# Kernel optimization log

Hardware: AMD Instinct MI355X
Metric: run time of the kernel (lower is better)

The kernel has to match this reference:

```python
import jax, jax.numpy as jnp
import numpy as np

EMBED_DIM = 256
NUM_HEADS = 8
HEAD_DIM = EMBED_DIM // NUM_HEADS


def setup_inputs() -> dict:
    key0 = jax.random.key(0)
    ks = jax.random.split(key0, 12)
    B, T, S, E = 4, 256, 16384, EMBED_DIM
    inv = 1.0 / np.sqrt(E)
    inputs = {
        "query": jax.random.normal(ks[0], (B, T, E), dtype=jnp.float32),
        "key": jax.random.normal(ks[1], (B, S, E), dtype=jnp.float32),
        "value": jax.random.normal(ks[2], (B, S, E), dtype=jnp.float32),
        "mask": jax.random.uniform(ks[3], (B, T, S), dtype=jnp.float32),
        # nn.MultiheadAttention in-projection (split into q/k/v parts) and out-projection
        "Wq": jax.random.uniform(ks[4], (E, E), jnp.float32, -inv, inv),
        "bq": jnp.zeros((E,), jnp.float32),
        "Wk": jax.random.uniform(ks[5], (E, E), jnp.float32, -inv, inv),
        "bk": jnp.zeros((E,), jnp.float32),
        "Wv": jax.random.uniform(ks[6], (E, E), jnp.float32, -inv, inv),
        "bv": jnp.zeros((E,), jnp.float32),
        "Wo": jax.random.uniform(ks[7], (E, E), jnp.float32, -inv, inv),
        "bo": jnp.zeros((E,), jnp.float32),
        # fixed default scaling factors (num_heads must be 8)
        "scaling_factors": jnp.asarray([32.0, 32.0, 16.0, 16.0, 8.0, 8.0, 4.0, 4.0], jnp.float32),
    }
    return inputs


def reference(query, key, value, mask, Wq, bq, Wk, bk, Wv, bv, Wo, bo, scaling_factors):
    B, T, E = query.shape
    S = key.shape[1]
    H, D = NUM_HEADS, HEAD_DIM
    # input projections (torch Linear convention: x @ W.T + b)
    q = (query @ Wq.T + bq).reshape(B, T, H, D).transpose(0, 2, 1, 3)  # [B,H,T,D]
    k = (key @ Wk.T + bk).reshape(B, S, H, D).transpose(0, 2, 1, 3)    # [B,H,S,D]
    v = (value @ Wv.T + bv).reshape(B, S, H, D).transpose(0, 2, 1, 3)  # [B,H,S,D]
    scale = 1.0 / jnp.sqrt(jnp.asarray(D, query.dtype))
    scores = jnp.einsum("bhtd,bhsd->bhts", q * scale, k)               # [B,H,T,S]
    # per-head scaled soft mask added as attention bias
    bias = mask[:, None, :, :] * scaling_factors[None, :, None, None]  # [B,H,T,S]
    attn = jax.nn.softmax(scores + bias, axis=-1)
    out = jnp.einsum("bhts,bhsd->bhtd", attn, v)                       # [B,H,T,D]
    out = out.transpose(0, 2, 1, 3).reshape(B, T, E)
    return out @ Wo.T + bo
```

## Files before the change

kernel.cpp:

```cpp
#include <hip/hip_runtime.h>

#define B_ 4
#define T_ 256
#define S_ 16384
#define E_ 256
#define H_ 8
#define D_ 32

typedef _Float16 f16;
typedef _Float16 f16x2 __attribute__((ext_vector_type(2)));
typedef _Float16 f16x4 __attribute__((ext_vector_type(4)));
typedef _Float16 f16x8 __attribute__((ext_vector_type(8)));
typedef float f32x4 __attribute__((ext_vector_type(4)));

typedef const __attribute__((address_space(1))) void* gas_t;
typedef __attribute__((address_space(3))) void* las_t;

#define FENCE() asm volatile("" ::: "memory")

__device__ __forceinline__ void gload_lds16(const void* g, void* l) {
    __builtin_amdgcn_global_load_lds((gas_t)g, (las_t)l, 16, 0, 0);
}

__device__ __forceinline__ f16x2 cvt_pk_f16(float a, float b) {
    return __builtin_bit_cast(f16x2, __builtin_amdgcn_cvt_pkrtz(a, b));
}

__device__ __forceinline__ f16x8 pack8(float4 a, float4 b) {
    f16x2 p0 = cvt_pk_f16(a.x, a.y), p1 = cvt_pk_f16(a.z, a.w);
    f16x2 p2 = cvt_pk_f16(b.x, b.y), p3 = cvt_pk_f16(b.z, b.w);
    return (f16x8){p0[0], p0[1], p1[0], p1[1], p2[0], p2[1], p3[0], p3[1]};
}

#define LOG2E 1.4426950408889634f

template <bool OUT16>
__device__ __forceinline__ void qproj32_body(
    f16* SMEM, const float* __restrict__ in, const float* __restrict__ w,
    const float* __restrict__ bias, void* __restrict__ outp, int bid, float oscale)
{
    f16 (*As)[264] = (f16(*)[264])SMEM;
    f16 (*Bs)[264] = (f16(*)[264])(SMEM + 32 * 264);
    int tid = threadIdx.x;
    int wq = tid >> 6, ln = tid & 63, g = ln >> 4, lc = ln & 15;
    int row0 = (bid & 31) * 32;
    int n0 = (bid >> 5) * 32;
    {
        int r = tid >> 3, q0 = (tid & 7) * 32;
        const float* ip = in + (size_t)(row0 + r) * 256 + q0;
        #pragma unroll
        for (int i = 0; i < 4; i++) {
            float4 v0 = *(const float4*)(ip + i * 8);
            float4 v1 = *(const float4*)(ip + i * 8 + 4);
            *(f16x8*)&As[r][q0 + i * 8] = pack8(v0, v1);
        }
        const float* wp = w + (size_t)(n0 + r) * 256 + q0;
        #pragma unroll
        for (int i = 0; i < 4; i++) {
            float4 v0 = *(const float4*)(wp + i * 8);
            float4 v1 = *(const float4*)(wp + i * 8 + 4);
            *(f16x8*)&Bs[r][q0 + i * 8] = pack8(v0, v1);
        }
    }
    __syncthreads();
    int mi = wq >> 1, ni = wq & 1;
    f32x4 acc = {0.f, 0.f, 0.f, 0.f};
    #pragma unroll
    for (int ks = 0; ks < 8; ks++) {
        f16x8 a = *(const f16x8*)&As[mi * 16 + lc][ks * 32 + g * 8];
        f16x8 bf = *(const f16x8*)&Bs[ni * 16 + lc][ks * 32 + g * 8];
        acc = __builtin_amdgcn_mfma_f32_16x16x32_f16(a, bf, acc, 0, 0, 0);
    }
    int n = n0 + ni * 16 + lc;
    float bv = bias[n];
    #pragma unroll
    for (int r = 0; r < 4; r++) {
        int row = row0 + mi * 16 + g * 4 + r;
        float val = (acc[r] + bv) * oscale;
        if (OUT16) ((f16*)outp)[(size_t)row * 256 + n] = (f16)val;
        else       ((float*)outp)[(size_t)row * 256 + n] = val;
    }
}

__global__ __launch_bounds__(256) void pre_kernel(
    const float* __restrict__ Wk, const float* __restrict__ Wv,
    f16* __restrict__ Wk16, f16* __restrict__ Wv16,
    const float* __restrict__ query, const float* __restrict__ Wq,
    const float* __restrict__ bq, f16* __restrict__ q16, float qscale)
{
    __shared__ __align__(16) f16 SMEM[16896];
    int bx = blockIdx.x;
    if (bx < 128) {
        const float* src = bx < 64 ? Wk : Wv;
        f16* dst = bx < 64 ? Wk16 : Wv16;
        int i = ((bx & 63) * 256 + threadIdx.x) * 4;
        float4 v = *(const float4*)(src + i);
        f16x4 h = {(f16)v.x, (f16)v.y, (f16)v.z, (f16)v.w};
        *(f16x4*)(dst + i) = h;
    } else {
        qproj32_body<true>(SMEM, query, Wq, bq, q16, bx - 128, qscale);
    }
}

template <int MODE>
__device__ __forceinline__ void proj8_body(
    char* SMEM, const float* __restrict__ in, const f16* __restrict__ w16,
    const float* __restrict__ bias, f16* __restrict__ out, int bx)
{
    f16 (*As)[128][40] = (f16(*)[128][40])SMEM;
    f16* Bs = (f16*)(SMEM + 20480);
    int tid = threadIdx.x;
    int wq = tid >> 6, ln = tid & 63, g = ln >> 4, lc = ln & 15;
    int mh = wq >> 2, nq = wq & 3;
    int row0 = bx * 128;

    f32x4 acc[4][4];
    #pragma unroll
    for (int i = 0; i < 4; i++)
        #pragma unroll
        for (int j = 0; j < 4; j++) acc[i][j] = (f32x4){0.f, 0.f, 0.f, 0.f};

    int am = tid >> 2, akq = (tid & 3) << 3;
    const float* abase = in + (size_t)(row0 + am) * 256 + akq;

    float4 Ar[2][2];
    auto issueA = [&](int t) {
        const float* p = abase + t * 32;
        Ar[t & 1][0] = *(const float4*)p;
        Ar[t & 1][1] = *(const float4*)(p + 4);
    };
    auto wrA = [&](int t) {
        *(f16x8*)&As[t & 1][am][akq] = pack8(Ar[t & 1][0], Ar[t & 1][1]);
    };
    auto issueB = [&](int t) {
        int kb = t * 32;
        #pragma unroll
        for (int c2 = 0; c2 < 2; c2++) {
            int cc = wq * 2 + c2;
            int row = cc * 16 + (ln >> 2);
            int sj = (ln & 3) ^ ((row >> 1) & 3);
            gload_lds16(w16 + (size_t)row * 256 + kb + sj * 8,
                        (char*)Bs + (t & 1) * 16384 + cc * 1024);
        }
    };

    issueB(0);
    FENCE();
    issueA(0); issueA(1);
    FENCE();

    #pragma unroll
    for (int t = 0; t < 8; t++) {
        if (t < 7) { asm volatile("s_waitcnt vmcnt(2)" ::: "memory"); }
        else       { asm volatile("s_waitcnt vmcnt(0)" ::: "memory"); }
        wrA(t);
        asm volatile("s_waitcnt lgkmcnt(0)" ::: "memory");
        __builtin_amdgcn_s_barrier();
        FENCE();
        if (t + 1 < 8) { issueB(t + 1); FENCE(); }
        if (t + 2 < 8) { issueA(t + 2); FENCE(); }

        f16x8 af[4], bf[4];
        #pragma unroll
        for (int mi = 0; mi < 4; mi++)
            af[mi] = *(const f16x8*)&As[t & 1][mh * 64 + mi * 16 + lc][g * 8];
        #pragma unroll
        for (int ni = 0; ni < 4; ni++) {
            int n = nq * 64 + ni * 16 + lc;
            bf[ni] = *(const f16x8*)&Bs[(t & 1) * 8192 + n * 32 + ((g ^ ((n >> 1) & 3)) << 3)];
        }
        #pragma unroll
        for (int mi = 0; mi < 4; mi++)
            #pragma unroll
            for (int ni = 0; ni < 4; ni++)
                acc[mi][ni] = __builtin_amdgcn_mfma_f32_16x16x32_f16(af[mi], bf[ni], acc[mi][ni], 0, 0, 0);
    }

    if (MODE == 1) {
        f16 (*TR)[264] = (f16(*)[264])SMEM;
        #pragma unroll
        for (int p = 0; p < 2; p++) {
            __syncthreads();
            if (mh == p) {
                #pragma unroll
                for (int ni = 0; ni < 4; ni++) {
                    int n = nq * 64 + ni * 16 + lc;
                    float bv = bias[n];
                    #pragma unroll
                    for (int mi = 0; mi < 4; mi++)
                        #pragma unroll
                        for (int r = 0; r < 4; r++)
                            TR[mi * 16 + g * 4 + r][n] = (f16)(acc[mi][ni][r] + bv);
                }
            }
            __syncthreads();
            int r = tid >> 3, c = tid & 7;
            f16* op = out + (size_t)(row0 + p * 64 + r) * 256 + c * 32;
            #pragma unroll
            for (int i = 0; i < 4; i++)
                *(f16x8*)(op + i * 8) = *(const f16x8*)&TR[r][c * 32 + i * 8];
        }
    } else {
        f16 (*TR)[68] = (f16(*)[68])SMEM;
        int bb = row0 >> 14, sbase = row0 & 16383;
        #pragma unroll
        for (int p = 0; p < 2; p++) {
            __syncthreads();
            if (mh == p) {
                #pragma unroll
                for (int ni = 0; ni < 4; ni++) {
                    int n = nq * 64 + ni * 16 + lc;
                    float bv = bias[n];
                    #pragma unroll
                    for (int mi = 0; mi < 4; mi++) {
                        f16x4 hv;
                        #pragma unroll
                        for (int r = 0; r < 4; r++) hv[r] = (f16)(acc[mi][ni][r] + bv);
                        *(f16x4*)&TR[n][mi * 16 + g * 4] = hv;
                    }
                }
            }
            __syncthreads();
            int n = tid >> 1, hf = tid & 1;
            f16* op = out + (((size_t)(bb * 256 + n)) << 14) + sbase + p * 64 + hf * 32;
            #pragma unroll
            for (int i = 0; i < 4; i++)
                *(f16x8*)(op + i * 8) = *(const f16x8*)&TR[n][hf * 32 + i * 8];
        }
    }
}

__global__ __launch_bounds__(512, 2) void proj_kv8(
    const float* __restrict__ key, const float* __restrict__ value,
    const f16* __restrict__ Wk16, const f16* __restrict__ Wv16,
    const float* __restrict__ bk, const float* __restrict__ bv,
    f16* __restrict__ k16, f16* __restrict__ v16T)
{
    __shared__ __align__(16) char SMEM[53248];
    int bx = blockIdx.x;
    if (bx < 512) proj8_body<1>(SMEM, key,   Wk16, bk, k16,  bx);
    else          proj8_body<2>(SMEM, value, Wv16, bv, v16T, bx - 512);
}

__global__ __launch_bounds__(256, 4) void out_proj(
    const float* __restrict__ in, const float* __restrict__ w,
    const float* __restrict__ bias, float* __restrict__ outp)
{
    __shared__ __align__(16) f16 SMEM[16896];
    qproj32_body<false>(SMEM, in, w, bias, outp, blockIdx.x + blockIdx.y * 32, 1.0f);
}

__global__ __launch_bounds__(1024, 4) void attn_kernel(
    const f16* __restrict__ q16,
    const f16* __restrict__ k16,
    const f16* __restrict__ v16T,
    const float* __restrict__ mask,
    const float* __restrict__ scal,
    float* __restrict__ partO, float* __restrict__ partL)
{
    constexpr int ITERS = 16;
    __shared__ __align__(16) f16 KT[3][32 * 256];
    __shared__ __align__(16) f16 VT[3][256 * 32];
    __shared__ __align__(16) float MT[3][128 * 32];

    int raw = blockIdx.x;
    int th = raw >> 7, b = (raw >> 5) & 3, ck = raw & 31;
    int tid = threadIdx.x;
    int wv = tid >> 6;
    int h = wv & 7, tsub = wv >> 3;
    int ln = tid & 63, g = ln >> 4, lc = ln & 15;
    int t0 = th * 128, s0 = ck * 512;

    float sc_h = scal[h] * LOG2E;
    float negfix = -(sc_h + 4.0f);

    f16x8 qf[4];
    #pragma unroll
    for (int tl = 0; tl < 4; tl++) {
        const f16* qp = q16 + (size_t)(b * T_ + t0 + tsub * 64 + tl * 16 + lc) * E_ + h * 32 + g * 8;
        qf[tl] = *(const f16x8*)qp;
    }

    f32x4 oac[4][2];
    float l_part[4];
    #pragma unroll
    for (int tl = 0; tl < 4; tl++) {
        oac[tl][0] = (f32x4){0.f, 0.f, 0.f, 0.f};
        oac[tl][1] = (f32x4){0.f, 0.f, 0.f, 0.f};
        l_part[tl] = 0.f;
    }

    auto stage = [&](int it, int bufi) {
        int sg0 = s0 + it * 32;
        {
            int sl = wv * 2 + (ln >> 5);
            int slot = (sl ^ (sl >> 3)) & 7;
            int jc = (ln & 31) ^ slot;
            gload_lds16(k16 + (size_t)(b * S_ + sg0 + sl) * E_ + jc * 8,
                        (char*)&KT[bufi][0] + wv * 1024);
        }
        {
            int dl = wv * 16 + (ln >> 2);
            int srcj = (ln & 3) ^ ((dl >> 1) & 3);
            gload_lds16(v16T + (size_t)(b * E_ + dl) * S_ + sg0 + srcj * 8,
                        (char*)&VT[bufi][0] + wv * 1024);
        }
        {
            int r = ln >> 3;
            int sj = (ln & 7) ^ r;
            gload_lds16(mask + (size_t)(b * T_ + t0 + wv * 8 + r) * S_ + sg0 + sj * 4,
                        (char*)&MT[bufi][0] + wv * 1024);
        }
    };

    stage(0, 0);
    stage(1, 1);

    f32x4 zero4 = {0.f, 0.f, 0.f, 0.f};
    int ib = 0;

    #pragma unroll 1
    for (int it = 0; it < ITERS; it++) {
        if (it + 1 < ITERS) { asm volatile("s_waitcnt vmcnt(3)" ::: "memory"); }
        else                { asm volatile("s_waitcnt vmcnt(0)" ::: "memory"); }
        __builtin_amdgcn_s_barrier();
        FENCE();
        if (it + 2 < ITERS) {
            int wb = ib + 2; if (wb >= 3) wb -= 3;
            stage(it + 2, wb);
        }

        f16x8 kb[2];
        #pragma unroll
        for (int si = 0; si < 2; si++) {
            int sl = si * 16 + lc;
            int slot = (sl ^ (sl >> 3)) & 7;
            int j = (h * 4 + g) ^ slot;
            kb[si] = *(const f16x8*)((char*)&KT[ib][0] + sl * 512 + j * 16);
        }
        f16x4 va[2][2];
        #pragma unroll
        for (int si = 0; si < 2; si++) {
            #pragma unroll
            for (int ni = 0; ni < 2; ni++) {
                int d = h * 32 + ni * 16 + lc;
                int u = (si * 2 + (g >> 1)) ^ ((d >> 1) & 3);
                va[si][ni] = *(const f16x4*)((char*)&VT[ib][0] + d * 64 + u * 16 + (g & 1) * 8);
            }
        }

        #pragma unroll
        for (int tl = 0; tl < 4; tl++) {
            int t = tsub * 64 + tl * 16 + lc;
            const float4 mf0 = *(const float4*)((char*)&MT[ib][0] + t * 128 + (((g    ) ^ (t & 7)) << 4));
            const float4 mf1 = *(const float4*)((char*)&MT[ib][0] + t * 128 + (((4 + g) ^ (t & 7)) << 4));
            f32x4 st0 = __builtin_amdgcn_mfma_f32_16x16x32_f16(kb[0], qf[tl], zero4, 0, 0, 0);
            f32x4 st1 = __builtin_amdgcn_mfma_f32_16x16x32_f16(kb[1], qf[tl], zero4, 0, 0, 0);
            float p0 = __builtin_amdgcn_exp2f(st0[0] + __builtin_fmaf(mf0.x, sc_h, negfix));
            float p1 = __builtin_amdgcn_exp2f(st0[1] + __builtin_fmaf(mf0.y, sc_h, negfix));
            float p2 = __builtin_amdgcn_exp2f(st0[2] + __builtin_fmaf(mf0.z, sc_h, negfix));
            float p3 = __builtin_amdgcn_exp2f(st0[3] + __builtin_fmaf(mf0.w, sc_h, negfix));
            float p4 = __builtin_amdgcn_exp2f(st1[0] + __builtin_fmaf(mf1.x, sc_h, negfix));
            float p5 = __builtin_amdgcn_exp2f(st1[1] + __builtin_fmaf(mf1.y, sc_h, negfix));
            float p6 = __builtin_amdgcn_exp2f(st1[2] + __builtin_fmaf(mf1.z, sc_h, negfix));
            float p7 = __builtin_amdgcn_exp2f(st1[3] + __builtin_fmaf(mf1.w, sc_h, negfix));
            l_part[tl] += ((p0 + p1) + (p2 + p3)) + ((p4 + p5) + (p6 + p7));
            f16x2 c01 = cvt_pk_f16(p0, p1);
            f16x2 c23 = cvt_pk_f16(p2, p3);
            f16x2 c45 = cvt_pk_f16(p4, p5);
            f16x2 c67 = cvt_pk_f16(p6, p7);
            f16x4 pb0 = {c01[0], c01[1], c23[0], c23[1]};
            f16x4 pb1 = {c45[0], c45[1], c67[0], c67[1]};
            oac[tl][0] = __builtin_amdgcn_mfma_f32_16x16x16f16(va[0][0], pb0, oac[tl][0], 0, 0, 0);
            oac[tl][0] = __builtin_amdgcn_mfma_f32_16x16x16f16(va[1][0], pb1, oac[tl][0], 0, 0, 0);
            oac[tl][1] = __builtin_amdgcn_mfma_f32_16x16x16f16(va[0][1], pb0, oac[tl][1], 0, 0, 0);
            oac[tl][1] = __builtin_amdgcn_mfma_f32_16x16x16f16(va[1][1], pb1, oac[tl][1], 0, 0, 0);
        }
        ib++; if (ib >= 3) ib -= 3;
    }

    #pragma unroll
    for (int tl = 0; tl < 4; tl++) {
        float lv = l_part[tl];
        lv += __shfl_xor(lv, 16, 64);
        lv += __shfl_xor(lv, 32, 64);
        l_part[tl] = lv;
    }
    float* po = partO + (size_t)raw * 128 * 256;
    #pragma unroll
    for (int tl = 0; tl < 4; tl++) {
        #pragma unroll
        for (int ni = 0; ni < 2; ni++) {
            float4 o4 = {oac[tl][ni][0], oac[tl][ni][1], oac[tl][ni][2], oac[tl][ni][3]};
            *(float4*)(po + (size_t)(tsub * 64 + tl * 16 + lc) * 256 + h * 32 + ni * 16 + g * 4) = o4;
        }
    }
    if (g == 0) {
        float* pl = partL + (size_t)raw * 128 * 8;
        #pragma unroll
        for (int tl = 0; tl < 4; tl++) {
            int trow = tsub * 64 + tl * 16 + lc;
            pl[trow * 8 + h] = l_part[tl];
        }
    }
}

__global__ __launch_bounds__(256) void combine_kernel(
    const float* __restrict__ partO, const float* __restrict__ partL,
    float* __restrict__ attnO)
{
    int bid = blockIdx.x;
    int b = bid >> 8, t = bid & 255;
    int th = t >> 7, tl = t & 127;
    int tid = threadIdx.x;
    __shared__ float sl[32][8];
    {
        int ck = tid >> 3, hh = tid & 7;
        size_t blk = (size_t)(th * 128 + b * 32 + ck);
        sl[ck][hh] = partL[blk * 1024 + tl * 8 + hh];
    }
    __syncthreads();
    int h = tid >> 5;
    float L = 0.f;
    #pragma unroll 8
    for (int ck = 0; ck < 32; ck++) L += sl[ck][h];
    float acc = 0.f;
    #pragma unroll 4
    for (int ck = 0; ck < 32; ck++) {
        size_t blk = (size_t)(th * 128 + b * 32 + ck);
        acc += partO[blk * 32768 + (size_t)tl * 256 + tid];
    }
    attnO[(size_t)bid * 256 + tid] = acc / L;
}

extern "C" void kernel_launch(void* const* d_in, const int* in_sizes, int n_in,
                              void* d_out, int out_size, void* d_ws, size_t ws_size,
                              hipStream_t stream) {
    (void)in_sizes; (void)n_in; (void)out_size; (void)ws_size;
    const float* query = (const float*)d_in[0];
    const float* key   = (const float*)d_in[1];
    const float* value = (const float*)d_in[2];
    const float* mask  = (const float*)d_in[3];
    const float* Wq = (const float*)d_in[4];
    const float* bq = (const float*)d_in[5];
    const float* Wk = (const float*)d_in[6];
    const float* bk = (const float*)d_in[7];
    const float* Wv = (const float*)d_in[8];
    const float* bv = (const float*)d_in[9];
    const float* Wo = (const float*)d_in[10];
    const float* bo = (const float*)d_in[11];
    const float* scal = (const float*)d_in[12];

    char* ws = (char*)d_ws;
    f16* Wk16 = (f16*)(ws + 0);
    f16* Wv16 = (f16*)(ws + (1 << 17));
    f16* q16  = (f16*)(ws + (4 << 17));
    float* attnO = (float*)(ws + 1048576);
    f16* k16  = (f16*)(ws + 2097152);
    f16* v16T = (f16*)(ws + 35651584);
    float* partO = (float*)(ws + 69206016);
    float* partL = (float*)(ws + 103809024);

    const float qscale = 0.17677669529663687f * LOG2E;
    pre_kernel<<<384, 256, 0, stream>>>(Wk, Wv, Wk16, Wv16, query, Wq, bq, q16, qscale);

    proj_kv8<<<1024, 512, 0, stream>>>(key, value, Wk16, Wv16, bk, bv, k16, v16T);

    attn_kernel<<<256, 1024, 0, stream>>>(q16, k16, v16T, mask, scal, partO, partL);
    combine_kernel<<<1024, 256, 0, stream>>>(partO, partL, attnO);

    out_proj<<<dim3(32, 8), 256, 0, stream>>>(attnO, Wo, bo, (float*)d_out);
}
```

Measured before the change: 135.6 us.

## Stream fp32 K/V activations straight into LDS with a triple-buffered pipeline

The K/V projection kernel no longer loads fp32 activations into registers and converts them to fp16 before storing to LDS. It now copies the fp32 tiles directly into swizzled LDS with global_load_lds and converts to fp16 while building the MFMA fragments. Both operands now go through a three-stage LDS ring with a single barrier per k-step. This frees registers and takes the conversion off the load-wait path, but LDS per block grows from 52 KB to 96 KB, which can reduce how many blocks fit on each CU.

```diff
diff --git a/kernel.cpp b/kernel.cpp
--- a/kernel.cpp
+++ b/kernel.cpp
@@ -29,6 +29,12 @@
 __device__ __forceinline__ f16x8 pack8(float4 a, float4 b) {
     f16x2 p0 = cvt_pk_f16(a.x, a.y), p1 = cvt_pk_f16(a.z, a.w);
     f16x2 p2 = cvt_pk_f16(b.x, b.y), p3 = cvt_pk_f16(b.z, b.w);
+    return (f16x8){p0[0], p0[1], p1[0], p1[1], p2[0], p2[1], p3[0], p3[1]};
+}
+
+__device__ __forceinline__ f16x8 pack8v(f32x4 a, f32x4 b) {
+    f16x2 p0 = cvt_pk_f16(a[0], a[1]), p1 = cvt_pk_f16(a[2], a[3]);
+    f16x2 p2 = cvt_pk_f16(b[0], b[1]), p3 = cvt_pk_f16(b[2], b[3]);
     return (f16x8){p0[0], p0[1], p1[0], p1[1], p2[0], p2[1], p3[0], p3[1]};
 }
 
@@ -103,77 +109,78 @@
 }
 
 template <int MODE>
-__device__ __forceinline__ void proj8_body(
+__device__ __forceinline__ void proj9_body(
     char* SMEM, const float* __restrict__ in, const f16* __restrict__ w16,
     const float* __restrict__ bias, f16* __restrict__ out, int bx)
 {
-    f16 (*As)[128][40] = (f16(*)[128][40])SMEM;
-    f16* Bs = (f16*)(SMEM + 20480);
+    char* Ab = SMEM;
+    char* Bb = SMEM + 49152;
     int tid = threadIdx.x;
     int wq = tid >> 6, ln = tid & 63, g = ln >> 4, lc = ln & 15;
     int mh = wq >> 2, nq = wq & 3;
     int row0 = bx * 128;
 
-    f32x4 acc[4][4];
-    #pragma unroll
-    for (int i = 0; i < 4; i++)
-        #pragma unroll
-        for (int j = 0; j < 4; j++) acc[i][j] = (f32x4){0.f, 0.f, 0.f, 0.f};
-
-    int am = tid >> 2, akq = (tid & 3) << 3;
-    const float* abase = in + (size_t)(row0 + am) * 256 + akq;
-
-    float4 Ar[2][2];
-    auto issueA = [&](int t) {
-        const float* p = abase + t * 32;
-        Ar[t & 1][0] = *(const float4*)p;
-        Ar[t & 1][1] = *(const float4*)(p + 4);
-    };
-    auto wrA = [&](int t) {
-        *(f16x8*)&As[t & 1][am][akq] = pack8(Ar[t & 1][0], Ar[t & 1][1]);
-    };
-    auto issueB = [&](int t) {
-        int kb = t * 32;
+    auto stage = [&](int t, int buf) {
         #pragma unroll
         for (int c2 = 0; c2 < 2; c2++) {
             int cc = wq * 2 + c2;
             int row = cc * 16 + (ln >> 2);
             int sj = (ln & 3) ^ ((row >> 1) & 3);
-            gload_lds16(w16 + (size_t)row * 256 + kb + sj * 8,
-                        (char*)Bs + (t & 1) * 16384 + cc * 1024);
+            gload_lds16(w16 + (size_t)row * 256 + t * 32 + sj * 8,
+                        Bb + buf * 16384 + cc * 1024);
+        }
+        #pragma unroll
+        for (int q2 = 0; q2 < 2; q2++) {
+            int q = wq * 2 + q2;
+            int rl = ln >> 3;
+            int ssl = (ln & 7) ^ rl;
+            gload_lds16(in + (size_t)(row0 + q * 8 + rl) * 256 + t * 32 + ssl * 4,
+                        Ab + buf * 16384 + q * 1024);
         }
     };
 
-    issueB(0);
-    FENCE();
-    issueA(0); issueA(1);
-    FENCE();
-
-    #pragma unroll
+    f32x4 acc[4][4];
+    #pragma unroll
+    for (int i = 0; i < 4; i++)
+        #pragma unroll
+        for (int j = 0; j < 4; j++) acc[i][j] = (f32x4){0.f, 0.f, 0.f, 0.f};
+
+    stage(0, 0);
+    stage(1, 1);
+
+    int ib = 0;
+    #pragma unroll 1
     for (int t = 0; t < 8; t++) {
-        if (t < 7) { asm volatile("s_waitcnt vmcnt(2)" ::: "memory"); }
+        if (t < 7) { asm volatile("s_waitcnt vmcnt(4)" ::: "memory"); }
         else       { asm volatile("s_waitcnt vmcnt(0)" ::: "memory"); }
-        wrA(t);
-        asm volatile("s_waitcnt lgkmcnt(0)" ::: "memory");
         __builtin_amdgcn_s_barrier();
         FENCE();
-        if (t + 1 < 8) { issueB(t + 1); FENCE(); }
-        if (t + 2 < 8) { issueA(t + 2); FENCE(); }
+        if (t + 2 < 8) {
+            int wb = ib + 2; if (wb >= 3) wb -= 3;
+            stage(t + 2, wb);
+        }
 
         f16x8 af[4], bf[4];
         #pragma unroll
-        for (int mi = 0; mi < 4; mi++)
-            af[mi] = *(const f16x8*)&As[t & 1][mh * 64 + mi * 16 + lc][g * 8];
+        for (int mi = 0; mi < 4; mi++) {
+            int row = mh * 64 + mi * 16 + lc;
+            int s0 = (2 * g) ^ (row & 7);
+            int s1 = (2 * g + 1) ^ (row & 7);
+            f32x4 lo = *(const f32x4*)(Ab + ib * 16384 + row * 128 + s0 * 16);
+            f32x4 hi = *(const f32x4*)(Ab + ib * 16384 + row * 128 + s1 * 16);
+            af[mi] = pack8v(lo, hi);
+        }
         #pragma unroll
         for (int ni = 0; ni < 4; ni++) {
             int n = nq * 64 + ni * 16 + lc;
-            bf[ni] = *(const f16x8*)&Bs[(t & 1) * 8192 + n * 32 + ((g ^ ((n >> 1) & 3)) << 3)];
+            bf[ni] = *(const f16x8*)(Bb + ib * 16384 + n * 64 + ((g ^ ((n >> 1) & 3)) << 4));
         }
         #pragma unroll
         for (int mi = 0; mi < 4; mi++)
             #pragma unroll
             for (int ni = 0; ni < 4; ni++)
                 acc[mi][ni] = __builtin_amdgcn_mfma_f32_16x16x32_f16(af[mi], bf[ni], acc[mi][ni], 0, 0, 0);
+        ib++; if (ib >= 3) ib -= 3;
     }
 
     if (MODE == 1) {
@@ -230,16 +237,16 @@
     }
 }
 
-__global__ __launch_bounds__(512, 2) void proj_kv8(
+__global__ __launch_bounds__(512, 2) void proj_kv9(
     const float* __restrict__ key, const float* __restrict__ value,
     const f16* __restrict__ Wk16, const f16* __restrict__ Wv16,
     const float* __restrict__ bk, const float* __restrict__ bv,
     f16* __restrict__ k16, f16* __restrict__ v16T)
 {
-    __shared__ __align__(16) char SMEM[53248];
+    __shared__ __align__(16) char SMEM[98304];
     int bx = blockIdx.x;
-    if (bx < 512) proj8_body<1>(SMEM, key,   Wk16, bk, k16,  bx);
-    else          proj8_body<2>(SMEM, value, Wv16, bv, v16T, bx - 512);
+    if (bx < 512) proj9_body<1>(SMEM, key,   Wk16, bk, k16,  bx);
+    else          proj9_body<2>(SMEM, value, Wv16, bv, v16T, bx - 512);
 }
 
 __global__ __launch_bounds__(256, 4) void out_proj(
@@ -464,7 +471,7 @@
     const float qscale = 0.17677669529663687f * LOG2E;
     pre_kernel<<<384, 256, 0, stream>>>(Wk, Wv, Wk16, Wv16, query, Wq, bq, q16, qscale);
 
-    proj_kv8<<<1024, 512, 0, stream>>>(key, value, Wk16, Wv16, bk, bv, k16, v16T);
+    proj_kv9<<<1024, 512, 0, stream>>>(key, value, Wk16, Wv16, bk, bv, k16, v16T);
 
     attn_kernel<<<256, 1024, 0, stream>>>(q16, k16, v16T, mask, scal, partO, partL);
     combine_kernel<<<1024, 256, 0, stream>>>(partO, partL, attnO);
```

After: 134.2 us. Within noise of the previous version (-1.1%).
